# Kernel tuning notes

Measured on AMD Instinct MI355X. Metric: run time of the kernel, lower is better.

Reference implementation:

```python
import math
import jax, jax.numpy as jnp
import numpy as np

B, L, DM = 2, 1024, 1024
STATE, EXPAND, CONV, DTR = 16, 2, 4, 8
INNER = DM * EXPAND          # 2048
NFFT = L // 2 + 1            # 513


def _silu(v):
    return v * jax.nn.sigmoid(v)


def setup_inputs() -> dict:
    key = jax.random.key(0)
    ks = jax.random.split(key, 12)
    s = lambda k, shape, sc=0.02: (jax.random.normal(k, shape, jnp.float32) * sc)
    # dt_proj bias initialized like the torch module: exp(U(0,1)*(log dt_max - log dt_min) + log dt_min)
    inv_dt = jnp.exp(jax.random.uniform(ks[10], (INNER,), jnp.float32)
                     * (math.log(0.1) - math.log(0.001)) + math.log(0.001))
    return {
        "x": jax.random.normal(ks[0], (B, L, DM), jnp.float32),
        "in_proj_w": s(ks[1], (2 * INNER, DM)),
        "conv_w": s(ks[2], (INNER, 1, CONV), 0.1),      # depthwise conv kernel
        "conv_b": jnp.zeros((INNER,), jnp.float32),
        "A_log": jnp.tile(jnp.log(jnp.arange(1, STATE + 1, dtype=jnp.float32)), (INNER, 1)),
        "D": jnp.ones((INNER,), jnp.float32),
        "x_proj_w": s(ks[3], (DTR + 2 * STATE, INNER)),
        "dt_proj_w": s(ks[4], (INNER, DTR)),
        "dt_proj_b": inv_dt,
        "filter_real": s(ks[5], (INNER, NFFT)),
        "filter_imag": s(ks[6], (INNER, NFFT)),
        "spectral_decay": jnp.ones((INNER,), jnp.float32) * 0.01,
        "fusion_w": s(ks[7], (INNER, 2 * INNER)),
        "fusion_b": jnp.zeros((INNER,), jnp.float32),
        "out_proj_w": s(ks[8], (DM, INNER)),
        "ln_gamma": jnp.ones((DM,), jnp.float32),
        "ln_beta": jnp.zeros((DM,), jnp.float32),
    }


def reference(x, in_proj_w, conv_w, conv_b, A_log, D, x_proj_w, dt_proj_w, dt_proj_b,
              filter_real, filter_imag, spectral_decay, fusion_w, fusion_b,
              out_proj_w, ln_gamma, ln_beta):
    residual = x
    xz = x @ in_proj_w.T                                   # [B,L,2*INNER]
    x_inner, z = xz[..., :INNER], xz[..., INNER:]
    z = _silu(z)

    # ---- SSM path ----
    xc = jnp.swapaxes(x_inner, 1, 2)                       # [B,E,L]
    xc = jax.lax.conv_general_dilated(
        xc, conv_w, (1,), [(CONV - 1, 0)],                 # causal depthwise conv (pad-left == torch pad + truncate)
        dimension_numbers=("NCH", "OIH", "NCH"),
        feature_group_count=INNER) + conv_b[None, :, None]
    x_conv = jnp.swapaxes(_silu(xc), 1, 2)                 # [B,L,E]

    x_dbc = x_conv @ x_proj_w.T                            # [B,L,DTR+2S]
    dt_x = x_dbc[..., :DTR]
    Bm = x_dbc[..., DTR:DTR + STATE]                       # [B,L,S]
    Cm = x_dbc[..., DTR + STATE:]                          # [B,L,S]
    dt = jax.nn.softplus(dt_x @ dt_proj_w.T + dt_proj_b)   # [B,L,E]
    A = -jnp.exp(A_log)                                    # [E,S]
    dA = jnp.exp(dt[..., None] * A)                        # [B,L,E,S]
    dBx = (dt * x_conv)[..., None] * Bm[:, :, None, :]     # [B,L,E,S]

    def step(h, inp):
        dA_t, dBx_t, C_t = inp
        h = dA_t * h + dBx_t                               # [B,E,S]
        return h, jnp.einsum('bes,bs->be', h, C_t)

    h0 = jnp.zeros((B, INNER, STATE), x.dtype)
    _, ys = jax.lax.scan(step, h0,
                         (jnp.swapaxes(dA, 0, 1), jnp.swapaxes(dBx, 0, 1), jnp.swapaxes(Cm, 0, 1)))
    y_ssm = jnp.swapaxes(ys, 0, 1) + x_conv * D            # [B,L,E]

    # ---- Spectral path ----
    xf = jnp.fft.rfft(jnp.swapaxes(x_inner, 1, 2), axis=-1)        # [B,E,NFFT]
    freqs = jnp.linspace(0.0, 1.0, NFFT)
    filt = (filter_real + 1j * filter_imag) * jnp.exp(-spectral_decay[:, None] * freqs[None, :])
    y_spec = jnp.swapaxes(jnp.fft.irfft(xf * filt[None], n=L, axis=-1), 1, 2)  # [B,L,E]

    # ---- Gated fusion ----
    g = jax.nn.sigmoid(jnp.concatenate([y_ssm, y_spec], -1) @ fusion_w.T + fusion_b)
    y = g * y_ssm + (1.0 - g) * y_spec
    y = y * z
    out = y @ out_proj_w.T + residual                      # [B,L,DM]

    mu = out.mean(-1, keepdims=True)
    var = out.var(-1, keepdims=True)
    return (out - mu) / jnp.sqrt(var + 1e-5) * ln_gamma + ln_beta
```

## Files before the change

kernel.cpp:

```cpp
#include <hip/hip_runtime.h>
#include <math.h>

#define B_ 2
#define L_ 1024
#define DM_ 1024
#define STATE_ 16
#define CONV_ 4
#define DTR_ 8
#define INNER_ 2048
#define M_ (B_*L_)
#define MD_ (B_*INNER_)
#define NFFT_ 513
#define NFP_ 1088
#define NCH_ 32
#define CHL_ 32
#define SK_ 16
#define KSL_ (2048/SK_)

typedef unsigned short u16;
typedef __attribute__((ext_vector_type(8))) short short8;
typedef __attribute__((ext_vector_type(8))) __bf16 bf16x8;
typedef __attribute__((ext_vector_type(4))) float f32x4;

__device__ __forceinline__ float frcp_(float x) { return __builtin_amdgcn_rcpf(x); }
__device__ __forceinline__ float fexp_(float x) { return __expf(x); }
__device__ __forceinline__ float fsigm_(float x) { return frcp_(1.f + __expf(-x)); }
__device__ __forceinline__ float fsilu_(float x) { return x * frcp_(1.f + __expf(-x)); }
__device__ __forceinline__ float fsoftplus_(float v) {
  return (v > 20.f) ? v : __logf(1.f + __expf(v));
}
__device__ __forceinline__ u16 f2bf(float f) {
  union { float f; unsigned u; } v; v.f = f;
  unsigned r = v.u + 0x7fffu + ((v.u >> 16) & 1u);
  return (u16)(r >> 16);
}
__device__ __forceinline__ float bf2f(u16 h) {
  union { unsigned u; float f; } v; v.u = ((unsigned)h) << 16;
  return v.f;
}
__device__ __forceinline__ void gload16(const void* g, void* l) {
  __builtin_amdgcn_global_load_lds(
      (const __attribute__((address_space(1))) unsigned*)g,
      (__attribute__((address_space(3))) unsigned*)l, 16, 0, 0);
}
__device__ __forceinline__ f32x4 mfma_bf16(short8 a, short8 b, f32x4 c) {
  return __builtin_amdgcn_mfma_f32_16x16x32_bf16(
      __builtin_bit_cast(bf16x8, a), __builtin_bit_cast(bf16x8, b), c, 0, 0, 0);
}

#define CVT_N0 2097152
#define CVT_N1 6291456
#define CVT_N2 14680064
#define CVT_NT 16777216
__global__ __launch_bounds__(256) void cvt4_k(
    const float* __restrict__ s0, const float* __restrict__ s1,
    const float* __restrict__ s2, const float* __restrict__ s3,
    u16* __restrict__ out)
{
  int i = (blockIdx.x*256 + threadIdx.x) * 4;
  const float* src; int off;
  if (i < CVT_N0)      { src = s0; off = 0; }
  else if (i < CVT_N1) { src = s1; off = CVT_N0; }
  else if (i < CVT_N2) { src = s2; off = CVT_N1; }
  else                 { src = s3; off = CVT_N2; }
  float4 v = *(const float4*)(src + (i - off));
  ushort4 o;
  o.x = f2bf(v.x); o.y = f2bf(v.y); o.z = f2bf(v.z); o.w = f2bf(v.w);
  *(ushort4*)(out + i) = o;
}

__device__ __forceinline__ void conv_body(int idx, const float* __restrict__ xz,
    const float* __restrict__ cw, const float* __restrict__ cb,
    float* __restrict__ xc)
{
  int c = idx & (INNER_-1);
  int g = idx >> 11;
  int b = g >> 7;
  int lb = (g & 127) * 8;
  float w0=cw[c*4+0], w1=cw[c*4+1], w2=cw[c*4+2], w3=cw[c*4+3];
  float bias = cb[c];
  float v[11];
  #pragma unroll
  for (int j = 0; j < 11; j++) {
    int l = lb - 3 + j;
    v[j] = (l >= 0) ? xz[((size_t)((b << 10) + l))*4096 + c] : 0.f;
  }
  #pragma unroll
  for (int j = 0; j < 8; j++) {
    float s = bias + w0*v[j] + w1*v[j+1] + w2*v[j+2] + w3*v[j+3];
    xc[((size_t)((b << 10) + lb + j))*INNER_ + c] = fsilu_(s);
  }
}

__device__ __forceinline__ void genWdft_body(int idx, u16* __restrict__ W)
{
  int l = idx & (L_-1);
  int col = idx >> 10;
  float v = 0.f;
  int f = col >> 1;
  if (f < NFFT_) {
    int ph = (l*f) & (L_-1);
    float th = (float)ph * (6.283185307179586f / (float)L_);
    v = (col & 1) ? -__sinf(th) : __cosf(th);
  }
  W[idx] = f2bf(v);
}

__device__ __forceinline__ void genWinv_body(int idx, u16* __restrict__ W)
{
  int r = idx % NFP_;
  int l = idx / NFP_;
  int f = r >> 1;
  float v = 0.f;
  if (f < NFFT_) {
    bool edge = (f == 0) || (f == 512);
    float sc = (edge ? 1.f : 2.f) / (float)L_;
    int ph = (f*l) & (L_-1);
    float th = (float)ph * (6.283185307179586f / (float)L_);
    if (r & 1) v = edge ? 0.f : -sc*__sinf(th);
    else       v = sc*__cosf(th);
  }
  W[idx] = f2bf(v);
}

__device__ __forceinline__ void xproj_body(int eb,
    const float* __restrict__ xconv, const float* __restrict__ W,
    float* __restrict__ part, void* lds)
{
  float (*Bs)[KSL_+4] = (float(*)[KSL_+4])lds;
  const int sk = eb & (SK_-1), mt = eb / SK_;
  const int k0 = sk*KSL_;
  for (int i = threadIdx.x; i < 40*KSL_; i += 256) {
    int n = i / KSL_, k = i & (KSL_-1);
    Bs[n][k] = W[(size_t)n*2048 + k0 + k];
  }
  __syncthreads();
  const int m = mt*256 + threadIdx.x;
  const float* arow = xconv + (size_t)m*2048 + k0;
  float acc[40];
  #pragma unroll
  for (int j=0;j<40;j++) acc[j]=0.f;
  for (int k = 0; k < KSL_; k += 4) {
    float4 a = *(const float4*)(arow + k);
    #pragma unroll
    for (int j = 0; j < 40; j++) {
      float4 b = *(const float4*)&Bs[j][k];
      acc[j] += a.x*b.x + a.y*b.y + a.z*b.z + a.w*b.w;
    }
  }
  float* o = part + ((size_t)sk*M_ + m)*40;
  #pragma unroll
  for (int j = 0; j < 10; j++)
    *(float4*)(o + j*4) = make_float4(acc[j*4], acc[j*4+1], acc[j*4+2], acc[j*4+3]);
}

template<int TM, int TN, int EPI, int YCH, int AUX>
__global__ __launch_bounds__((TM/64)*(TN/32)*64) void mgemm_k(
    const u16* __restrict__ Ab, const u16* __restrict__ Bb,
    void* __restrict__ Cout, int K, int ldc,
    const float* __restrict__ aux0, u16* __restrict__ aux1,
    const float* __restrict__ aux2, const float* __restrict__ aux3,
    int gx, int gy,
    const float* __restrict__ ga, const float* __restrict__ gb,
    const float* __restrict__ gc, float* __restrict__ go,
    u16* __restrict__ gw)
{
  constexpr int WN   = TN/32;
  constexpr int NW   = (TM/64)*WN;
  constexpr int NTHR = NW*64;
  __shared__ __align__(16) u16 As[2][TM*64];
  __shared__ __align__(16) u16 Bs[2][TN*64];
  const int t = threadIdx.x;

  if constexpr (AUX != 0) {
    int eb = (int)blockIdx.x - gx*gy;
    if (eb >= 0) {
      if constexpr (AUX == 1) {
        genWdft_body(eb*NTHR + t, gw);
      } else if constexpr (AUX == 2) {
        if (eb < 2048) conv_body(eb*256 + t, ga, gb, gc, go);
        else           genWinv_body((eb - 2048)*256 + t, gw);
      } else {
        xproj_body(eb, ga, gb, go, (void*)&As[0][0]);
      }
      return;
    }
  }

  const int lane = t & 63;
  const int w = t >> 6;
  const int wm = w / WN, wn = w % WN;

  const int nwg = gx * gy;
  const int bid = blockIdx.x;
  const int lid = (bid & 7) * (nwg >> 3) + (bid >> 3);
  int bx, by;
  if (YCH) { by = lid / gx; bx = lid - by*gx; }
  else     { bx = lid / gy; by = lid - bx*gy; }
  const int M0 = by * TM, N0 = bx * TN;

  f32x4 acc[4][2] = {};

  auto stage = [&](int buf, int k0) {
    #pragma unroll
    for (int q = 0; q < TM*8/NTHR; q++) {
      int u = q*NTHR + t;
      int row = u >> 3, gpr = u & 7;
      int grp = gpr ^ (row & 7);
      gload16(Ab + (size_t)(M0+row)*K + k0 + grp*8, &As[buf][u*8]);
    }
    #pragma unroll
    for (int q = 0; q < TN*8/NTHR; q++) {
      int u = q*NTHR + t;
      int row = u >> 3, gpr = u & 7;
      int grp = gpr ^ (row & 7);
      gload16(Bb + (size_t)(N0+row)*K + k0 + grp*8, &Bs[buf][u*8]);
    }
  };

  stage(0, 0);
  const int nk = K >> 6;
  for (int ks = 0; ks < nk; ks++) {
    const int buf = ks & 1;
    __syncthreads();
    if (ks + 1 < nk) stage(buf ^ 1, (ks + 1) << 6);
    const u16* Asb = As[buf];
    const u16* Bsb = Bs[buf];
    #pragma unroll
    for (int kk = 0; kk < 2; kk++) {
      const int quad = lane >> 4;
      const int grp = kk*4 + quad;
      short8 af[4], bfr[2];
      #pragma unroll
      for (int i = 0; i < 4; i++) {
        int row = wm*64 + i*16 + (lane & 15);
        af[i] = *(const short8*)&Asb[(row*8 + (grp ^ (row & 7)))*8];
      }
      #pragma unroll
      for (int j = 0; j < 2; j++) {
        int row = wn*32 + j*16 + (lane & 15);
        bfr[j] = *(const short8*)&Bsb[(row*8 + (grp ^ (row & 7)))*8];
      }
      #pragma unroll
      for (int i = 0; i < 4; i++)
        #pragma unroll
        for (int j = 0; j < 2; j++)
          acc[i][j] = mfma_bf16(af[i], bfr[j], acc[i][j]);
    }
  }

  #pragma unroll
  for (int i = 0; i < 4; i++) {
    int mbase = M0 + wm*64 + i*16 + (lane >> 4)*4;
    #pragma unroll
    for (int j = 0; j < 2; j++) {
      int n = N0 + wn*32 + j*16 + (lane & 15);
      #pragma unroll
      for (int r = 0; r < 4; r++) {
        int m = mbase + r;
        float v = acc[i][j][r];
        if (EPI == 0) {
          ((float*)Cout)[(size_t)m*ldc + n] = v;
        } else if (EPI == 1) {
          float g  = fsigm_(v + aux0[n]);
          float ys = bf2f(aux1[(size_t)m*4096 + n]);
          float yp = bf2f(aux1[(size_t)m*4096 + 2048 + n]);
          float z  = aux2[(size_t)m*4096 + 2048 + n];
          ((u16*)Cout)[(size_t)m*ldc + n] = f2bf((g*ys + (1.f-g)*yp)*fsilu_(z));
        } else if (EPI == 2) {
          ((float*)Cout)[(size_t)m*ldc + n] = v + aux2[(size_t)m*ldc + n];
        } else if (EPI == 3) {
          float pv = __shfl_xor(v, 1, 64);
          int f = n >> 1;
          float outv = 0.f;
          if (f < NFFT_) {
            int c = m & (INNER_-1);
            float d  = fexp_(-aux2[c] * (float)f * (1.f/512.f));
            float wr = aux0[c*NFFT_+f]*d, wi = aux3[c*NFFT_+f]*d;
            float a = (n & 1) ? pv : v;
            float b = (n & 1) ? v : pv;
            outv = (n & 1) ? (a*wi + b*wr) : (a*wr - b*wi);
          }
          ((u16*)Cout)[(size_t)m*ldc + n] = f2bf(outv);
        } else if (EPI == 5) {
          ((float*)Cout)[(size_t)m*ldc + n] = v;
          if (n < 2048) {
            int b2 = m >> 10, l2 = m & 1023;
            aux1[((size_t)(b2*2048 + n) << 10) + l2] = f2bf(v);
          }
        } else {
          int b2 = m >> 11, c2 = m & (INNER_-1);
          ((u16*)Cout)[((size_t)((b2 << 10) + n) << 12) + 2048 + c2] = f2bf(v);
        }
      }
    }
  }
}

__global__ __launch_bounds__(256) void xpred_k(const float* __restrict__ part,
                                               float* __restrict__ xdbc)
{
  int i = blockIdx.x*256 + threadIdx.x;
  float s = 0.f;
  #pragma unroll
  for (int sk = 0; sk < SK_; sk++) s += part[(size_t)sk*81920 + i];
  xdbc[i] = s;
}

__global__ __launch_bounds__(256) void scan1_k(
    const float* __restrict__ xdbc, const float* __restrict__ xconv,
    const float* __restrict__ A_log, const float* __restrict__ dtw,
    const float* __restrict__ dtb, float* __restrict__ Pq)
{
  int idx = blockIdx.x*256 + threadIdx.x;
  int e  = idx & (INNER_-1);
  int bc = idx >> 11;
  int ch = bc & (NCH_-1);
  int b  = bc >> 5;
  float A[STATE_];
  #pragma unroll
  for (int s=0;s<STATE_;s++) A[s] = -fexp_(A_log[e*STATE_+s]);
  float w[DTR_];
  #pragma unroll
  for (int r=0;r<DTR_;r++) w[r] = dtw[e*DTR_+r];
  float bias = dtb[e];
  float h[STATE_] = {};
  float sdt = 0.f;
  int mbase = b*L_ + ch*CHL_;
  float dtx[DTR_], Bv[STATE_], xcv;
  {
    const float* row = xdbc + (size_t)mbase*40;
    #pragma unroll
    for (int r=0;r<DTR_;r++) dtx[r] = row[r];
    #pragma unroll
    for (int s=0;s<STATE_;s++) Bv[s] = row[8+s];
    xcv = xconv[(size_t)mbase*INNER_ + e];
  }
  for (int l=0;l<CHL_;l++) {
    float ndtx[DTR_], nBv[STATE_], nxcv = 0.f;
    if (l+1 < CHL_) {
      const float* nrow = xdbc + (size_t)(mbase+l+1)*40;
      #pragma unroll
      for (int r=0;r<DTR_;r++) ndtx[r] = nrow[r];
      #pragma unroll
      for (int s=0;s<STATE_;s++) nBv[s] = nrow[8+s];
      nxcv = xconv[(size_t)(mbase+l+1)*INNER_ + e];
    } else {
      #pragma unroll
      for (int r=0;r<DTR_;r++) ndtx[r] = 0.f;
      #pragma unroll
      for (int s=0;s<STATE_;s++) nBv[s] = 0.f;
    }
    float v = bias;
    #pragma unroll
    for (int r=0;r<DTR_;r++) v += dtx[r]*w[r];
    float dt = fsoftplus_(v);
    sdt += dt;
    float dx = dt * xcv;
    #pragma unroll
    for (int s=0;s<STATE_;s++) {
      float dA = fexp_(dt*A[s]);
      h[s] = dA*h[s] + dx*Bv[s];
    }
    #pragma unroll
    for (int r=0;r<DTR_;r++) dtx[r] = ndtx[r];
    #pragma unroll
    for (int s=0;s<STATE_;s++) Bv[s] = nBv[s];
    xcv = nxcv;
  }
  float* o = Pq + (size_t)idx*32;
  #pragma unroll
  for (int s=0;s<STATE_;s++) { o[s] = fexp_(A[s]*sdt); o[16+s] = h[s]; }
}

__global__ __launch_bounds__(256) void scan2_k(float* __restrict__ Pq)
{
  int idx = blockIdx.x*256 + threadIdx.x;
  int s = idx & 15;
  int e = (idx >> 4) & (INNER_-1);
  int b = idx >> 15;
  float h = 0.f;
  for (int ch = 0; ch < NCH_; ch++) {
    size_t base = ((size_t)(b*NCH_+ch)*INNER_ + e)*32;
    float p = Pq[base + s];
    float q = Pq[base + 16 + s];
    Pq[base + 16 + s] = h;
    h = p*h + q;
  }
}

__global__ __launch_bounds__(256) void scan3_k(
    const float* __restrict__ xdbc, const float* __restrict__ xconv,
    const float* __restrict__ A_log, const float* __restrict__ dtw,
    const float* __restrict__ dtb, const float* __restrict__ Dp,
    const float* __restrict__ Pq, u16* __restrict__ ycat)
{
  int idx = blockIdx.x*256 + threadIdx.x;
  int e  = idx & (INNER_-1);
  int bc = idx >> 11;
  int ch = bc & (NCH_-1);
  int b  = bc >> 5;
  float A[STATE_];
  #pragma unroll
  for (int s=0;s<STATE_;s++) A[s] = -fexp_(A_log[e*STATE_+s]);
  float w[DTR_];
  #pragma unroll
  for (int r=0;r<DTR_;r++) w[r] = dtw[e*DTR_+r];
  float bias = dtb[e];
  float Dv = Dp[e];
  float h[STATE_];
  const float* hi = Pq + (size_t)idx*32 + 16;
  #pragma unroll
  for (int s=0;s<STATE_;s++) h[s] = hi[s];
  int mbase = b*L_ + ch*CHL_;
  float dtx[DTR_], Bv[STATE_], Cv[STATE_], xcv;
  {
    const float* row = xdbc + (size_t)mbase*40;
    #pragma unroll
    for (int r=0;r<DTR_;r++) dtx[r] = row[r];
    #pragma unroll
    for (int s=0;s<STATE_;s++) { Bv[s] = row[8+s]; Cv[s] = row[24+s]; }
    xcv = xconv[(size_t)mbase*INNER_ + e];
  }
  for (int l=0;l<CHL_;l++) {
    float ndtx[DTR_], nBv[STATE_], nCv[STATE_], nxcv = 0.f;
    if (l+1 < CHL_) {
      const float* nrow = xdbc + (size_t)(mbase+l+1)*40;
      #pragma unroll
      for (int r=0;r<DTR_;r++) ndtx[r] = nrow[r];
      #pragma unroll
      for (int s=0;s<STATE_;s++) { nBv[s] = nrow[8+s]; nCv[s] = nrow[24+s]; }
      nxcv = xconv[(size_t)(mbase+l+1)*INNER_ + e];
    } else {
      #pragma unroll
      for (int r=0;r<DTR_;r++) ndtx[r] = 0.f;
      #pragma unroll
      for (int s=0;s<STATE_;s++) { nBv[s] = 0.f; nCv[s] = 0.f; }
    }
    float v = bias;
    #pragma unroll
    for (int r=0;r<DTR_;r++) v += dtx[r]*w[r];
    float dt = fsoftplus_(v);
    float dx = dt * xcv;
    float y = 0.f;
    #pragma unroll
    for (int s=0;s<STATE_;s++) {
      float dA = fexp_(dt*A[s]);
      h[s] = dA*h[s] + dx*Bv[s];
      y += h[s]*Cv[s];
    }
    ycat[(size_t)(mbase+l)*4096 + e] = f2bf(y + xcv*Dv);
    #pragma unroll
    for (int r=0;r<DTR_;r++) dtx[r] = ndtx[r];
    #pragma unroll
    for (int s=0;s<STATE_;s++) { Bv[s] = nBv[s]; Cv[s] = nCv[s]; }
    xcv = nxcv;
  }
}

__global__ __launch_bounds__(256) void ln_k(const float* __restrict__ inp,
    const float* __restrict__ gma, const float* __restrict__ bta,
    float* __restrict__ out)
{
  int m = blockIdx.x;
  const float* row = inp + (size_t)m*DM_;
  float s=0.f, s2=0.f;
  float v[4];
  #pragma unroll
  for (int j=0;j<4;j++) {
    v[j] = row[threadIdx.x + j*256];
    s += v[j]; s2 += v[j]*v[j];
  }
  #pragma unroll
  for (int off=32; off>=1; off>>=1) {
    s  += __shfl_down(s, off);
    s2 += __shfl_down(s2, off);
  }
  __shared__ float rs[4], rs2[4], stats[2];
  int wid = threadIdx.x >> 6;
  if ((threadIdx.x & 63) == 0) { rs[wid]=s; rs2[wid]=s2; }
  __syncthreads();
  if (threadIdx.x == 0) {
    float ts  = rs[0]+rs[1]+rs[2]+rs[3];
    float ts2 = rs2[0]+rs2[1]+rs2[2]+rs2[3];
    float mu  = ts/(float)DM_;
    float var = ts2/(float)DM_ - mu*mu;
    stats[0] = mu; stats[1] = rsqrtf(var + 1e-5f);
  }
  __syncthreads();
  float mu = stats[0], rstd = stats[1];
  #pragma unroll
  for (int j=0;j<4;j++) {
    int n = threadIdx.x + j*256;
    out[(size_t)m*DM_ + n] = (v[j]-mu)*rstd*gma[n] + bta[n];
  }
}

extern "C" void kernel_launch(void* const* d_in, const int* in_sizes, int n_in,
                              void* d_out, int out_size, void* d_ws, size_t ws_size,
                              hipStream_t stream)
{
  const float* x       = (const float*)d_in[0];
  const float* in_w    = (const float*)d_in[1];
  const float* conv_w  = (const float*)d_in[2];
  const float* conv_b  = (const float*)d_in[3];
  const float* A_log   = (const float*)d_in[4];
  const float* Dp      = (const float*)d_in[5];
  const float* xproj_w = (const float*)d_in[6];
  const float* dt_w    = (const float*)d_in[7];
  const float* dt_b    = (const float*)d_in[8];
  const float* f_re    = (const float*)d_in[9];
  const float* f_im    = (const float*)d_in[10];
  const float* s_dec   = (const float*)d_in[11];
  const float* fus_w   = (const float*)d_in[12];
  const float* fus_b   = (const float*)d_in[13];
  const float* out_w   = (const float*)d_in[14];
  const float* ln_g    = (const float*)d_in[15];
  const float* ln_b    = (const float*)d_in[16];
  float* out = (float*)d_out;

  float* ws    = (float*)d_ws;
  float* xz    = ws;
  float* xconv = xz    + 8388608;
  float* xdbc  = xconv + 4194304;
  float* Pq    = xdbc  + 81920;
  u16* ub      = (u16*)(Pq + 4194304);
  u16* xb      = ub;
  u16* inwb    = xb    + 2097152;
  u16* fuswb   = inwb  + 4194304;
  u16* outwb   = fuswb + 8388608;
  u16* xt      = outwb + 2097152;
  u16* Wb      = xt    + 4194304;
  u16* XFb     = Wb    + 1114112;
  u16* ycat    = XFb   + 4456448;
  u16* ycomb   = xt;
  u16* Winv    = xb;
  float* outp  = xconv;
  float* part  = (float*)inwb;

  cvt4_k<<<CVT_NT/1024, 256, 0, stream>>>(x, in_w, fus_w, out_w, xb);

  mgemm_k<128,128,5,0,1><<<512 + (NFP_*1024)/512, 512, 0, stream>>>(
      xb, inwb, xz, 1024, 4096, nullptr, xt, nullptr, nullptr, 32, 16,
      nullptr, nullptr, nullptr, nullptr, Wb);
  mgemm_k<128,64,3,1,2><<<544 + 2048 + (1024*NFP_)/256, 256, 0, stream>>>(
      xt, Wb, XFb, 1024, NFP_, f_re, nullptr, s_dec, f_im, 17, 32,
      xz, conv_w, conv_b, xconv, Winv);
  mgemm_k<128,64,6,1,3><<<512 + SK_*8, 256, 0, stream>>>(
      XFb, Winv, ycat, NFP_, 0, nullptr, nullptr, nullptr, nullptr, 16, 32,
      xconv, xproj_w, nullptr, part, nullptr);
  xpred_k<<<(M_*40)/256, 256, 0, stream>>>(part, xdbc);
  scan1_k<<<(B_*NCH_*INNER_)/256, 256, 0, stream>>>(xdbc, xconv, A_log, dt_w, dt_b, Pq);
  scan2_k<<<(B_*INNER_*STATE_)/256, 256, 0, stream>>>(Pq);
  scan3_k<<<(B_*NCH_*INNER_)/256, 256, 0, stream>>>(xdbc, xconv, A_log, dt_w, dt_b, Dp, Pq, ycat);
  mgemm_k<128,64,1,0,0><<<512, 256, 0, stream>>>(
      ycat, fuswb, ycomb, 4096, 2048, fus_b, ycat, xz, nullptr, 32, 16,
      nullptr, nullptr, nullptr, nullptr, nullptr);
  mgemm_k<64,64,2,1,0><<<512, 128, 0, stream>>>(
      ycomb, outwb, outp, 2048, 1024, nullptr, nullptr, x, nullptr, 16, 32,
      nullptr, nullptr, nullptr, nullptr, nullptr);
  ln_k<<<M_, 256, 0, stream>>>(outp, ln_g, ln_b, out);
}
```

Measured before the change: 403.6 us.

## Split-K the fusion and out-proj GEMMs and hide weight casts inside GEMM launches

The fusion GEMM becomes a 128x128 split-K-by-2 GEMM that writes fp32 partials. A new elementwise kernel sums the partials and applies the gate, and the out-projection GEMM is also split-K-by-2, with its partials summed inside the layernorm kernel together with the residual. The bf16 conversion of the fusion and out-proj weights moves out of the upfront convert kernel into extra blocks of the earlier GEMM launches, so it overlaps with that work. The aim is more workgroups for the small GEMMs and a shorter serial convert. The cost is extra fp32 partial traffic and one additional kernel launch.

Measured after the change: 395.5 us. 1.02x faster.

```diff
diff --git a/kernel.cpp b/kernel.cpp
--- a/kernel.cpp
+++ b/kernel.cpp
@@ -48,25 +48,33 @@
       __builtin_bit_cast(bf16x8, a), __builtin_bit_cast(bf16x8, b), c, 0, 0, 0);
 }
 
-#define CVT_N0 2097152
-#define CVT_N1 6291456
-#define CVT_N2 14680064
-#define CVT_NT 16777216
-__global__ __launch_bounds__(256) void cvt4_k(
+#define CVT2_N0 2097152
+#define CVT2_NT 6291456
+__global__ __launch_bounds__(256) void cvt2_k(
     const float* __restrict__ s0, const float* __restrict__ s1,
-    const float* __restrict__ s2, const float* __restrict__ s3,
     u16* __restrict__ out)
 {
   int i = (blockIdx.x*256 + threadIdx.x) * 4;
   const float* src; int off;
-  if (i < CVT_N0)      { src = s0; off = 0; }
-  else if (i < CVT_N1) { src = s1; off = CVT_N0; }
-  else if (i < CVT_N2) { src = s2; off = CVT_N1; }
-  else                 { src = s3; off = CVT_N2; }
+  if (i < CVT2_N0) { src = s0; off = 0; }
+  else             { src = s1; off = CVT2_N0; }
   float4 v = *(const float4*)(src + (i - off));
   ushort4 o;
   o.x = f2bf(v.x); o.y = f2bf(v.y); o.z = f2bf(v.z); o.w = f2bf(v.w);
   *(ushort4*)(out + i) = o;
+}
+
+__device__ __forceinline__ void cvt16_body(int eb, int nthr, int t,
+    const float* __restrict__ src, u16* __restrict__ dst)
+{
+  int i = (eb*nthr + t)*16;
+  #pragma unroll
+  for (int q = 0; q < 4; q++) {
+    float4 v = *(const float4*)(src + i + q*4);
+    ushort4 o;
+    o.x = f2bf(v.x); o.y = f2bf(v.y); o.z = f2bf(v.z); o.w = f2bf(v.w);
+    *(ushort4*)(dst + i + q*4) = o;
+  }
 }
 
 __device__ __forceinline__ void conv_body(int idx, const float* __restrict__ xz,
@@ -154,7 +162,7 @@
     *(float4*)(o + j*4) = make_float4(acc[j*4], acc[j*4+1], acc[j*4+2], acc[j*4+3]);
 }
 
-template<int TM, int TN, int EPI, int YCH, int AUX>
+template<int TM, int TN, int EPI, int YCH, int AUX, int KS>
 __global__ __launch_bounds__((TM/64)*(TN/32)*64) void mgemm_k(
     const u16* __restrict__ Ab, const u16* __restrict__ Bb,
     void* __restrict__ Cout, int K, int ldc,
@@ -163,7 +171,8 @@
     int gx, int gy,
     const float* __restrict__ ga, const float* __restrict__ gb,
     const float* __restrict__ gc, float* __restrict__ go,
-    u16* __restrict__ gw)
+    u16* __restrict__ gw,
+    int ldk, const float* __restrict__ cvs, u16* __restrict__ cvd)
 {
   constexpr int WN   = TN/32;
   constexpr int NW   = (TM/64)*WN;
@@ -171,15 +180,18 @@
   __shared__ __align__(16) u16 As[2][TM*64];
   __shared__ __align__(16) u16 Bs[2][TN*64];
   const int t = threadIdx.x;
+  const int nwg = gx * gy;
 
   if constexpr (AUX != 0) {
-    int eb = (int)blockIdx.x - gx*gy;
+    int eb = (int)blockIdx.x - nwg*KS;
     if (eb >= 0) {
       if constexpr (AUX == 1) {
-        genWdft_body(eb*NTHR + t, gw);
+        if (eb < 2176) genWdft_body(eb*NTHR + t, gw);
+        else           cvt16_body(eb - 2176, NTHR, t, cvs, cvd);
       } else if constexpr (AUX == 2) {
-        if (eb < 2048) conv_body(eb*256 + t, ga, gb, gc, go);
-        else           genWinv_body((eb - 2048)*256 + t, gw);
+        if (eb < 2048)      conv_body(eb*256 + t, ga, gb, gc, go);
+        else if (eb < 6400) genWinv_body((eb - 2048)*256 + t, gw);
+        else                cvt16_body(eb - 6400, NTHR, t, cvs, cvd);
       } else {
         xproj_body(eb, ga, gb, go, (void*)&As[0][0]);
       }
@@ -191,8 +203,10 @@
   const int w = t >> 6;
   const int wm = w / WN, wn = w % WN;
 
-  const int nwg = gx * gy;
-  const int bid = blockIdx.x;
+  int bid = blockIdx.x;
+  int ks = 0;
+  if constexpr (KS > 1) { ks = bid / nwg; bid -= ks*nwg; }
+  const int k0 = ks * K;
   const int lid = (bid & 7) * (nwg >> 3) + (bid >> 3);
   int bx, by;
   if (YCH) { by = lid / gx; bx = lid - by*gx; }
@@ -201,29 +215,29 @@
 
   f32x4 acc[4][2] = {};
 
-  auto stage = [&](int buf, int k0) {
+  auto stage = [&](int buf, int kk0) {
     #pragma unroll
     for (int q = 0; q < TM*8/NTHR; q++) {
       int u = q*NTHR + t;
       int row = u >> 3, gpr = u & 7;
       int grp = gpr ^ (row & 7);
-      gload16(Ab + (size_t)(M0+row)*K + k0 + grp*8, &As[buf][u*8]);
+      gload16(Ab + (size_t)(M0+row)*ldk + k0 + kk0 + grp*8, &As[buf][u*8]);
     }
     #pragma unroll
     for (int q = 0; q < TN*8/NTHR; q++) {
       int u = q*NTHR + t;
       int row = u >> 3, gpr = u & 7;
       int grp = gpr ^ (row & 7);
-      gload16(Bb + (size_t)(N0+row)*K + k0 + grp*8, &Bs[buf][u*8]);
+      gload16(Bb + (size_t)(N0+row)*ldk + k0 + kk0 + grp*8, &Bs[buf][u*8]);
     }
   };
 
   stage(0, 0);
   const int nk = K >> 6;
-  for (int ks = 0; ks < nk; ks++) {
-    const int buf = ks & 1;
+  for (int kst = 0; kst < nk; kst++) {
+    const int buf = kst & 1;
     __syncthreads();
-    if (ks + 1 < nk) stage(buf ^ 1, (ks + 1) << 6);
+    if (kst + 1 < nk) stage(buf ^ 1, (kst + 1) << 6);
     const u16* Asb = As[buf];
     const u16* Bsb = Bs[buf];
     #pragma unroll
@@ -261,14 +275,6 @@
         float v = acc[i][j][r];
         if (EPI == 0) {
           ((float*)Cout)[(size_t)m*ldc + n] = v;
-        } else if (EPI == 1) {
-          float g  = fsigm_(v + aux0[n]);
-          float ys = bf2f(aux1[(size_t)m*4096 + n]);
-          float yp = bf2f(aux1[(size_t)m*4096 + 2048 + n]);
-          float z  = aux2[(size_t)m*4096 + 2048 + n];
-          ((u16*)Cout)[(size_t)m*ldc + n] = f2bf((g*ys + (1.f-g)*yp)*fsilu_(z));
-        } else if (EPI == 2) {
-          ((float*)Cout)[(size_t)m*ldc + n] = v + aux2[(size_t)m*ldc + n];
         } else if (EPI == 3) {
           float pv = __shfl_xor(v, 1, 64);
           int f = n >> 1;
@@ -288,13 +294,44 @@
             int b2 = m >> 10, l2 = m & 1023;
             aux1[((size_t)(b2*2048 + n) << 10) + l2] = f2bf(v);
           }
-        } else {
+        } else if (EPI == 6) {
           int b2 = m >> 11, c2 = m & (INNER_-1);
           ((u16*)Cout)[((size_t)((b2 << 10) + n) << 12) + 2048 + c2] = f2bf(v);
+        } else {
+          float* P = (float*)Cout + (size_t)ks * ((size_t)gy*TM*ldc);
+          P[(size_t)m*ldc + n] = v;
         }
       }
     }
   }
+}
+
+__global__ __launch_bounds__(256) void combine_gate_k(
+    const float* __restrict__ P, const float* __restrict__ fus_b,
+    const u16* __restrict__ ycat, const float* __restrict__ xz,
+    u16* __restrict__ ycomb)
+{
+  int i4 = (blockIdx.x*256 + threadIdx.x)*4;
+  int m = i4 >> 11, n = i4 & 2047;
+  float4 p0 = *(const float4*)(P + i4);
+  float4 p1 = *(const float4*)(P + 4194304 + i4);
+  ushort4 ysv = *(const ushort4*)(ycat + (size_t)m*4096 + n);
+  ushort4 ypv = *(const ushort4*)(ycat + (size_t)m*4096 + 2048 + n);
+  float4 zv = *(const float4*)(xz + (size_t)m*4096 + 2048 + n);
+  float4 fb = *(const float4*)(fus_b + n);
+  float pp[4] = {p0.x+p1.x, p0.y+p1.y, p0.z+p1.z, p0.w+p1.w};
+  float zz[4] = {zv.x, zv.y, zv.z, zv.w};
+  float bb[4] = {fb.x, fb.y, fb.z, fb.w};
+  u16 ys[4] = {ysv.x, ysv.y, ysv.z, ysv.w};
+  u16 yp[4] = {ypv.x, ypv.y, ypv.z, ypv.w};
+  ushort4 o;
+  u16* op = (u16*)&o;
+  #pragma unroll
+  for (int j = 0; j < 4; j++) {
+    float g = fsigm_(pp[j] + bb[j]);
+    op[j] = f2bf((g*bf2f(ys[j]) + (1.f-g)*bf2f(yp[j]))*fsilu_(zz[j]));
+  }
+  *(ushort4*)(ycomb + i4) = o;
 }
 
 __global__ __launch_bounds__(256) void xpred_k(const float* __restrict__ part,
@@ -458,17 +495,19 @@
   }
 }
 
-__global__ __launch_bounds__(256) void ln_k(const float* __restrict__ inp,
+__global__ __launch_bounds__(256) void ln2_k(const float* __restrict__ Q,
+    const float* __restrict__ xres,
     const float* __restrict__ gma, const float* __restrict__ bta,
     float* __restrict__ out)
 {
   int m = blockIdx.x;
-  const float* row = inp + (size_t)m*DM_;
   float s=0.f, s2=0.f;
   float v[4];
   #pragma unroll
   for (int j=0;j<4;j++) {
-    v[j] = row[threadIdx.x + j*256];
+    int n = threadIdx.x + j*256;
+    size_t idx = (size_t)m*DM_ + n;
+    v[j] = Q[idx] + Q[2097152 + idx] + xres[idx];
     s += v[j]; s2 += v[j]*v[j];
   }
   #pragma unroll
@@ -535,29 +574,32 @@
   u16* ycat    = XFb   + 4456448;
   u16* ycomb   = xt;
   u16* Winv    = xb;
-  float* outp  = xconv;
   float* part  = (float*)inwb;
-
-  cvt4_k<<<CVT_NT/1024, 256, 0, stream>>>(x, in_w, fus_w, out_w, xb);
-
-  mgemm_k<128,128,5,0,1><<<512 + (NFP_*1024)/512, 512, 0, stream>>>(
+  float* fpart = xconv;
+  float* opart = Pq;
+
+  cvt2_k<<<CVT2_NT/1024, 256, 0, stream>>>(x, in_w, xb);
+
+  mgemm_k<128,128,5,0,1,1><<<512 + 2176 + 1024, 512, 0, stream>>>(
       xb, inwb, xz, 1024, 4096, nullptr, xt, nullptr, nullptr, 32, 16,
-      nullptr, nullptr, nullptr, nullptr, Wb);
-  mgemm_k<128,64,3,1,2><<<544 + 2048 + (1024*NFP_)/256, 256, 0, stream>>>(
+      nullptr, nullptr, nullptr, nullptr, Wb, 1024, fus_w, fuswb);
+  mgemm_k<128,64,3,1,2,1><<<544 + 2048 + 4352 + 512, 256, 0, stream>>>(
       xt, Wb, XFb, 1024, NFP_, f_re, nullptr, s_dec, f_im, 17, 32,
-      xz, conv_w, conv_b, xconv, Winv);
-  mgemm_k<128,64,6,1,3><<<512 + SK_*8, 256, 0, stream>>>(
+      xz, conv_w, conv_b, xconv, Winv, 1024, out_w, outwb);
+  mgemm_k<128,64,6,1,3,1><<<512 + SK_*8, 256, 0, stream>>>(
       XFb, Winv, ycat, NFP_, 0, nullptr, nullptr, nullptr, nullptr, 16, 32,
-      xconv, xproj_w, nullptr, part, nullptr);
+      xconv, xproj_w, nullptr, part, nullptr, NFP_, nullptr, nullptr);
   xpred_k<<<(M_*40)/256, 256, 0, stream>>>(part, xdbc);
   scan1_k<<<(B_*NCH_*INNER_)/256, 256, 0, stream>>>(xdbc, xconv, A_log, dt_w, dt_b, Pq);
   scan2_k<<<(B_*INNER_*STATE_)/256, 256, 0, stream>>>(Pq);
   scan3_k<<<(B_*NCH_*INNER_)/256, 256, 0, stream>>>(xdbc, xconv, A_log, dt_w, dt_b, Dp, Pq, ycat);
-  mgemm_k<128,64,1,0,0><<<512, 256, 0, stream>>>(
-      ycat, fuswb, ycomb, 4096, 2048, fus_b, ycat, xz, nullptr, 32, 16,
-      nullptr, nullptr, nullptr, nullptr, nullptr);
-  mgemm_k<64,64,2,1,0><<<512, 128, 0, stream>>>(
-      ycomb, outwb, outp, 2048, 1024, nullptr, nullptr, x, nullptr, 16, 32,
-      nullptr, nullptr, nullptr, nullptr, nullptr);
-  ln_k<<<M_, 256, 0, stream>>>(outp, ln_g, ln_b, out);
-}
+  mgemm_k<128,128,7,0,0,2><<<2*256, 512, 0, stream>>>(
+      ycat, fuswb, fpart, 2048, 2048, nullptr, nullptr, nullptr, nullptr, 16, 16,
+      nullptr, nullptr, nullptr, nullptr, nullptr, 4096, nullptr, nullptr);
+  combine_gate_k<<<(2048*2048/4)/256, 256, 0, stream>>>(
+      fpart, fus_b, ycat, xz, ycomb);
+  mgemm_k<64,64,7,1,0,2><<<2*512, 128, 0, stream>>>(
+      ycomb, outwb, opart, 1024, 1024, nullptr, nullptr, nullptr, nullptr, 16, 32,
+      nullptr, nullptr, nullptr, nullptr, nullptr, 2048, nullptr, nullptr);
+  ln2_k<<<M_, 256, 0, stream>>>(opart, x, ln_g, ln_b, out);
+}
```
